# Kernel tuning notes

Hardware: AMD Instinct MI355X
Metric: run time of the kernel (lower is better)

Reference implementation:

```python
import jax, jax.numpy as jnp
import numpy as np

B, C_IN, C_OUT, H, W = 16, 128, 256, 80, 80
K, STRIDE, PAD = 3, 2, 1
KK = K * K
HO = (H + 2 * PAD - K) // STRIDE + 1
WO = (W + 2 * PAD - K) // STRIDE + 1


def setup_inputs() -> dict:
    key = jax.random.key(0)
    ks = jax.random.split(key, 3)
    x = jax.random.normal(ks[0], (B, C_IN, H, W), jnp.float32)
    offset_w = jax.random.normal(ks[1], (2 * KK, C_IN), jnp.float32) * 0.01
    offset_b = jnp.zeros((2 * KK,), jnp.float32)
    deform_w = jax.random.normal(ks[2], (C_OUT, C_IN, K, K), jnp.float32) * (1.0 / np.sqrt(C_IN * KK))
    deform_b = jnp.zeros((C_OUT,), jnp.float32)
    bn_gamma = jnp.ones((C_OUT,), jnp.float32)
    bn_beta = jnp.zeros((C_OUT,), jnp.float32)
    return dict(x=x, offset_w=offset_w, offset_b=offset_b, deform_w=deform_w,
                deform_b=deform_b, bn_gamma=bn_gamma, bn_beta=bn_beta)


def _bilinear_gather(x, py, px):
    # x: [B,C,H,W]; py,px: [B,KK,HO,WO] float sample coords; zero-pad outside.
    Bb, C, Hh, Ww = x.shape
    y0 = jnp.floor(py)
    x0 = jnp.floor(px)
    wy1 = py - y0
    wx1 = px - x0
    y0i = y0.astype(jnp.int32)
    x0i = x0.astype(jnp.int32)
    flat = x.reshape(Bb, C, Hh * Ww)

    def gather(yi, xi):
        valid = (yi >= 0) & (yi < Hh) & (xi >= 0) & (xi < Ww)
        idx = jnp.clip(yi, 0, Hh - 1) * Ww + jnp.clip(xi, 0, Ww - 1)
        g = jax.vmap(lambda f, i: f[:, i])(flat, idx.reshape(Bb, -1))
        g = g.reshape(Bb, C, *yi.shape[1:])
        return g * valid[:, None].astype(x.dtype)

    g00 = gather(y0i, x0i)
    g01 = gather(y0i, x0i + 1)
    g10 = gather(y0i + 1, x0i)
    g11 = gather(y0i + 1, x0i + 1)
    wy1 = wy1[:, None]  # [B,1,KK,HO,WO]
    wx1 = wx1[:, None]
    wy0 = 1.0 - wy1
    wx0 = 1.0 - wx1
    return wy0 * (wx0 * g00 + wx1 * g01) + wy1 * (wx0 * g10 + wx1 * g11)


def reference(x, offset_w, offset_b, deform_w, deform_b, bn_gamma, bn_beta):
    Bb = x.shape[0]
    # offset conv: 1x1, stride 2 (H,W even -> simple subsample)
    xs = x[:, :, ::2, ::2]  # [B,C,HO,WO]
    off = jnp.einsum('oc,bchw->bohw', offset_w, xs) + offset_b[None, :, None, None]
    off = off.reshape(Bb, KK, 2, HO, WO)  # torchvision layout: (dy,dx) per kernel tap
    dy, dx = off[:, :, 0], off[:, :, 1]
    ky = (jnp.arange(KK) // K).astype(jnp.float32)
    kx = (jnp.arange(KK) % K).astype(jnp.float32)
    base_y = (jnp.arange(HO) * STRIDE - PAD).astype(jnp.float32)
    base_x = (jnp.arange(WO) * STRIDE - PAD).astype(jnp.float32)
    py = base_y[None, None, :, None] + ky[None, :, None, None] + dy
    px = base_x[None, None, None, :] + kx[None, :, None, None] + dx
    sampled = _bilinear_gather(x, py, px)  # [B,C,KK,HO,WO]
    w = deform_w.reshape(C_OUT, C_IN * KK)
    out = jnp.einsum('ok,bkhw->bohw', w, sampled.reshape(Bb, C_IN * KK, HO, WO))
    out = out + deform_b[None, :, None, None]
    # BatchNorm2d in training mode (batch stats, biased var, eps=1e-5)
    mean = out.mean(axis=(0, 2, 3))
    var = out.var(axis=(0, 2, 3))
    out = (out - mean[None, :, None, None]) * jax.lax.rsqrt(var + 1e-5)[None, :, None, None]
    out = out * bn_gamma[None, :, None, None] + bn_beta[None, :, None, None]
    # SiLU
    return out * jax.nn.sigmoid(out)
```

## Files before the change

### kernel.cpp

```cpp
#include <hip/hip_runtime.h>
#include <hip/hip_bf16.h>

#define B_    16
#define CIN_  128
#define COUT_ 256
#define H_    80
#define W_    80
#define HO_   40
#define WO_   40
#define KK_   9
#define SK_   1152
#define NPIX_ 25600
#define NKS_  36

typedef __attribute__((ext_vector_type(8))) short short8;
typedef __attribute__((ext_vector_type(4))) float floatx4;

__device__ __forceinline__ unsigned short f2bu(float v) {
  __hip_bfloat16 h = __float2bfloat16(v);
  return *reinterpret_cast<unsigned short*>(&h);
}
__device__ __forceinline__ float bu2f(unsigned short u) {
  return __uint_as_float(((unsigned)u) << 16);
}
__device__ __forceinline__ unsigned int pk2(float a, float b) {
  return (unsigned)f2bu(a) | ((unsigned)f2bu(b) << 16);
}
__device__ __forceinline__ void gl_lds16(const unsigned short* g, unsigned short* l) {
  __builtin_amdgcn_global_load_lds(
      (const __attribute__((address_space(1))) unsigned int*)(const void*)g,
      (__attribute__((address_space(3))) unsigned int*)(void*)l, 16, 0, 0);
}

__global__ __launch_bounds__(256) void k_pack(const float* __restrict__ dw,
                                              unsigned short* __restrict__ Apk) {
  int t = blockIdx.x * 256 + threadIdx.x;
  int j  = t & 7;
  int qd = (t >> 3) & 3;
  int m  = (t >> 5) & 255;
  int ks = t >> 13;
  int k  = ks * 32 + qd * 8 + j;
  int kk = k >> 7, ci = k & 127;
  Apk[t] = f2bu(dw[m * SK_ + ci * KK_ + kk]);
}

__global__ __launch_bounds__(256) void k_cl(const float* __restrict__ x,
                                            const float* __restrict__ ow,
                                            const float* __restrict__ ob,
                                            unsigned short* __restrict__ xcl,
                                            float* __restrict__ off) {
  __shared__ unsigned int ts[CIN_ * 41];
  __shared__ float owl[18 * CIN_];
  __shared__ float obl[18];
  const int tid = threadIdx.x;
  const int bid = blockIdx.x;
  const int xcd = bid & 7;
  const int i0_ = bid >> 3;
  const int b   = (i0_ / 80) * 8 + xcd;
  const int y   = i0_ % 80;
  const bool even = (y & 1) == 0;

  for (int j = tid; j < CIN_ * 20; j += 256) {
    int ci = j / 20, xq = j % 20;
    float4 v = *(const float4*)&x[(((size_t)b * CIN_ + ci) * H_ + y) * W_ + xq * 4];
    ts[ci * 41 + xq * 2 + 0] = pk2(v.x, v.y);
    ts[ci * 41 + xq * 2 + 1] = pk2(v.z, v.w);
  }
  if (even) {
    for (int j = tid; j < 18 * CIN_; j += 256) owl[j] = ow[j];
    if (tid < 18) obl[tid] = ob[tid];
  }
  __syncthreads();

  unsigned short* op = xcl + ((size_t)b * H_ * W_ + (size_t)y * W_) * CIN_;
  for (int j = tid; j < 40 * 32; j += 256) {
    int xw = j >> 5, cg = j & 31;
    unsigned w0 = ts[(cg * 4 + 0) * 41 + xw];
    unsigned w1 = ts[(cg * 4 + 1) * 41 + xw];
    unsigned w2 = ts[(cg * 4 + 2) * 41 + xw];
    unsigned w3 = ts[(cg * 4 + 3) * 41 + xw];
    uint2 lo = make_uint2((w0 & 0xFFFFu) | (w1 << 16),
                          (w2 & 0xFFFFu) | (w3 << 16));
    uint2 hi = make_uint2((w0 >> 16) | (w1 & 0xFFFF0000u),
                          (w2 >> 16) | (w3 & 0xFFFF0000u));
    *(uint2*)(op + (size_t)(2 * xw) * CIN_ + cg * 4)     = lo;
    *(uint2*)(op + (size_t)(2 * xw + 1) * CIN_ + cg * 4) = hi;
  }

  if (even) {
    const int ho = y >> 1;
    for (int i = tid; i < 18 * WO_; i += 256) {
      int o = i / WO_, wo = i - o * WO_;
      float acc = obl[o];
      const float* wr = &owl[o * CIN_];
#pragma unroll 4
      for (int ci = 0; ci < CIN_; ci++)
        acc += wr[ci] * bu2f((unsigned short)(ts[ci * 41 + wo] & 0xFFFFu));
      off[((b * 18 + o) * HO_ + ho) * WO_ + wo] = acc;
    }
  }
}

__global__ __launch_bounds__(256) void k_sample_cl(const unsigned short* __restrict__ xcl,
                                                   const float* __restrict__ off,
                                                   unsigned short* __restrict__ Spk) {
  __shared__ __align__(16) int   pidx[80 * 4];
  __shared__ __align__(16) float pw[80 * 4];
  const int tid = threadIdx.x;
  const int j0   = blockIdx.x;
  const int xcd  = j0 & 7;
  const int s    = j0 >> 3;
  const int b_hi = s / 180;
  const int t0   = s % 180;
  const int g    = t0 / 9;
  const int kk   = t0 % 9;
  const int b    = b_hi * 8 + xcd;
  const int ho0  = g * 2;

  if (tid < 80) {
    int hop = tid / 40, px = tid % 40;
    int ho = ho0 + hop;
    float dy = off[((b * 18 + 2 * kk) * HO_ + ho) * WO_ + px];
    float dx = off[((b * 18 + 2 * kk + 1) * HO_ + ho) * WO_ + px];
    float py  = (float)(2 * ho - 1 + (kk / 3)) + dy;
    float pxf = (float)(2 * px - 1 + (kk % 3)) + dx;
    float y0f = floorf(py), x0f = floorf(pxf);
    float wy1 = py - y0f, wx1 = pxf - x0f;
    float wy0 = 1.f - wy1, wx0 = 1.f - wx1;
    int y0 = (int)y0f, x0 = (int)x0f;
    int y1 = y0 + 1, x1 = x0 + 1;
    bool vy0 = (y0 >= 0) && (y0 < H_);
    bool vy1 = (y1 >= 0) && (y1 < H_);
    bool vx0 = (x0 >= 0) && (x0 < W_);
    bool vx1 = (x1 >= 0) && (x1 < W_);
    int y0c = min(max(y0, 0), H_ - 1), y1c = min(max(y1, 0), H_ - 1);
    int x0c = min(max(x0, 0), W_ - 1), x1c = min(max(x1, 0), W_ - 1);
    pidx[tid * 4 + 0] = (y0c * W_ + x0c) << 7;  pw[tid * 4 + 0] = (vy0 && vx0) ? wy0 * wx0 : 0.f;
    pidx[tid * 4 + 1] = (y0c * W_ + x1c) << 7;  pw[tid * 4 + 1] = (vy0 && vx1) ? wy0 * wx1 : 0.f;
    pidx[tid * 4 + 2] = (y1c * W_ + x0c) << 7;  pw[tid * 4 + 2] = (vy1 && vx0) ? wy1 * wx0 : 0.f;
    pidx[tid * 4 + 3] = (y1c * W_ + x1c) << 7;  pw[tid * 4 + 3] = (vy1 && vx1) ? wy1 * wx1 : 0.f;
  }
  __syncthreads();

  const unsigned short* xb = xcl + (size_t)b * (H_ * W_ * CIN_);
#pragma unroll
  for (int it = 0; it < 5; it++) {
    int i = it * 256 + tid;
    int oct = i & 15;
    int pxh = i >> 4;
    int4   I  = *(const int4*)&pidx[pxh * 4];
    float4 Wv = *(const float4*)&pw[pxh * 4];
    short8 c00 = *(const short8*)(xb + I.x + oct * 8);
    short8 c01 = *(const short8*)(xb + I.y + oct * 8);
    short8 c10 = *(const short8*)(xb + I.z + oct * 8);
    short8 c11 = *(const short8*)(xb + I.w + oct * 8);
    short8 r;
#pragma unroll
    for (int i2 = 0; i2 < 8; i2++) {
      float v = Wv.x * bu2f((unsigned short)c00[i2]) +
                Wv.y * bu2f((unsigned short)c01[i2]) +
                Wv.z * bu2f((unsigned short)c10[i2]) +
                Wv.w * bu2f((unsigned short)c11[i2]);
      r[i2] = (short)f2bu(v);
    }
    int p  = b * 1600 + (ho0 + (pxh / 40)) * 40 + (pxh % 40);
    int pt = p >> 4, lm = p & 15;
    int ks = kk * 4 + (oct >> 2);
    int qd = oct & 3;
    *(short8*)&Spk[(((size_t)pt * NKS_ + ks) * 64 + qd * 16 + lm) * 8] = r;
  }
}

__global__ __launch_bounds__(256) void k_gemm(const unsigned short* __restrict__ Apk,
                                              const unsigned short* __restrict__ Spk,
                                              float* __restrict__ c0,
                                              float* __restrict__ c1) {
  __shared__ __align__(16) unsigned short a_sh[2][2048];
  __shared__ __align__(16) unsigned short b_sh[2][2048];

  const int tid = threadIdx.x;
  const int wv = tid >> 6;
  const int ln = tid & 63;
  const int lm = ln & 15;
  const int qd = ln >> 4;

  const int bid = blockIdx.x;
  const int xcd = bid & 7;
  const int i   = bid >> 3;
  const int b   = xcd + 8 * (i / 200);
  const int r_  = i % 200;
  const int pxg = r_ >> 3;
  const int cq  = (r_ >> 1) & 3;
  const int ksp = r_ & 1;
  const int pt0 = b * 100 + pxg * 4;
  const int cbase = cq * 64;
  const int ks0 = ksp * 18;

  const unsigned short* agbase = Apk + (size_t)ks0 * 8192 + cbase * 32 + tid * 8;
  const unsigned short* bgbase = Spk + ((size_t)(pt0 + wv) * NKS_ + ks0) * 512 + ln * 8;

  floatx4 acc[4];
#pragma unroll
  for (int mt = 0; mt < 4; mt++) acc[mt] = (floatx4){0.f, 0.f, 0.f, 0.f};

  gl_lds16(agbase, &a_sh[0][0] + wv * 512);
  gl_lds16(bgbase, &b_sh[0][0] + wv * 512);
  __syncthreads();

  for (int ks = 0; ks < 18; ks++) {
    const int buf = ks & 1, nb = buf ^ 1;
    if (ks + 1 < 18) {
      gl_lds16(agbase + (size_t)(ks + 1) * 8192, &a_sh[nb][0] + wv * 512);
      gl_lds16(bgbase + (size_t)(ks + 1) * 512,  &b_sh[nb][0] + wv * 512);
    }
    const unsigned short* al = &a_sh[buf][0] + lm * 32 + qd * 8;
    const unsigned short* bl = &b_sh[buf][0] + wv * 512 + ln * 8;
    short8 a0 = *(const short8*)(al + 0 * 512);
    short8 a1 = *(const short8*)(al + 1 * 512);
    short8 a2 = *(const short8*)(al + 2 * 512);
    short8 a3 = *(const short8*)(al + 3 * 512);
    short8 bv = *(const short8*)(bl);
    acc[0] = __builtin_amdgcn_mfma_f32_16x16x32_bf16(a0, bv, acc[0], 0, 0, 0);
    acc[1] = __builtin_amdgcn_mfma_f32_16x16x32_bf16(a1, bv, acc[1], 0, 0, 0);
    acc[2] = __builtin_amdgcn_mfma_f32_16x16x32_bf16(a2, bv, acc[2], 0, 0, 0);
    acc[3] = __builtin_amdgcn_mfma_f32_16x16x32_bf16(a3, bv, acc[3], 0, 0, 0);
    __syncthreads();
  }

  const int p = (pt0 + wv) * 16 + lm;
  const int bb = p / 1600, rem = p % 1600;
  float* ob = (ksp ? c1 : c0) + (size_t)bb * COUT_ * 1600 + rem;
#pragma unroll
  for (int mt = 0; mt < 4; mt++) {
#pragma unroll
    for (int r = 0; r < 4; r++) {
      const int c = cbase + mt * 16 + qd * 4 + r;
      ob[(size_t)c * 1600] = acc[mt][r];
    }
  }
}

__global__ __launch_bounds__(256) void k_stats(const float* __restrict__ io0,
                                               const float* __restrict__ io1,
                                               float* __restrict__ accum) {
  const int c = blockIdx.x >> 2;
  const int q = blockIdx.x & 3;
  const int tid = threadIdx.x;
  float s1 = 0.f, s2 = 0.f;
  for (int i = q * (NPIX_ / 4) + tid; i < (q + 1) * (NPIX_ / 4); i += 256) {
    int b = i / 1600, r = i - b * 1600;
    size_t idx = ((size_t)b * COUT_ + c) * 1600 + r;
    float v = io0[idx] + io1[idx];
    s1 += v;
    s2 += v * v;
  }
#pragma unroll
  for (int d = 1; d < 64; d <<= 1) {
    s1 += __shfl_xor(s1, d, 64);
    s2 += __shfl_xor(s2, d, 64);
  }
  __shared__ float rs[4], rq[4];
  if ((tid & 63) == 0) { rs[tid >> 6] = s1; rq[tid >> 6] = s2; }
  __syncthreads();
  if (tid == 0) {
    atomicAdd(&accum[c],         rs[0] + rs[1] + rs[2] + rs[3]);
    atomicAdd(&accum[COUT_ + c], rq[0] + rq[1] + rq[2] + rq[3]);
  }
}

__global__ __launch_bounds__(256) void k_bn(float* __restrict__ io0,
                                            const float* __restrict__ io1,
                                            const float* __restrict__ accum,
                                            const float* __restrict__ gamma,
                                            const float* __restrict__ beta) {
  const int t = blockIdx.x * 256 + threadIdx.x;
  const int i0 = t * 4;
  const int c = (i0 / (HO_ * WO_)) % COUT_;
  const float mean = accum[c] * (1.f / NPIX_);
  const float var  = accum[COUT_ + c] * (1.f / NPIX_) - mean * mean;
  const float inv  = rsqrtf(var + 1e-5f);
  const float g  = gamma[c] * inv;
  const float be = beta[c] - mean * g;
  float4 r0 = *(const float4*)(io0 + i0);
  float4 r1 = *(const float4*)(io1 + i0);
  float v[4] = {r0.x + r1.x, r0.y + r1.y, r0.z + r1.z, r0.w + r1.w};
#pragma unroll
  for (int q = 0; q < 4; q++) {
    float u = v[q] * g + be;
    v[q] = u / (1.f + expf(-u));
  }
  *(float4*)(io0 + i0) = make_float4(v[0], v[1], v[2], v[3]);
}

extern "C" void kernel_launch(void* const* d_in, const int* in_sizes, int n_in,
                              void* d_out, int out_size, void* d_ws, size_t ws_size,
                              hipStream_t stream) {
  const float* x     = (const float*)d_in[0];
  const float* ow    = (const float*)d_in[1];
  const float* ob    = (const float*)d_in[2];
  const float* dw    = (const float*)d_in[3];
  const float* gamma = (const float*)d_in[5];
  const float* beta  = (const float*)d_in[6];
  float* out = (float*)d_out;

  float* off   = (float*)d_ws;
  float* accum = off + B_ * 18 * HO_ * WO_;
  unsigned short* Apk = (unsigned short*)(accum + 2 * COUT_);
  unsigned short* Spk = Apk + (size_t)SK_ * COUT_;
  unsigned short* xcl = Spk + (size_t)NPIX_ * SK_;
  float* c1 = (float*)xcl;

  hipMemsetAsync(accum, 0, 2 * COUT_ * sizeof(float), stream);
  k_pack<<<SK_, 256, 0, stream>>>(dw, Apk);
  k_cl<<<B_ * H_, 256, 0, stream>>>(x, ow, ob, xcl, off);
  k_sample_cl<<<B_ * KK_ * 20, 256, 0, stream>>>(xcl, off, Spk);
  k_gemm<<<3200, 256, 0, stream>>>(Apk, Spk, out, c1);
  k_stats<<<COUT_ * 4, 256, 0, stream>>>(out, c1, accum);
  k_bn<<<(NPIX_ * COUT_ / 4 + 255) / 256, 256, 0, stream>>>(
      out, c1, accum, gamma, beta);
}
```

Before: 195.2 us.

## Drop split-K, widen GEMM channel tile, fuse BN statistics into GEMM epilogue

The GEMM no longer splits K across two partial outputs. Each block now covers 128 output channels over the full K range, with 8 MFMA accumulators per wave, and the grid shrinks from 3200 to 800 blocks. The per-channel sum and sum-of-squares are reduced in the GEMM epilogue through shuffles, LDS atomics and global atomics, so the separate stats kernel and the second partial buffer go away. This removes a full read/write pass of the output and the partial-sum traffic, at the cost of fewer blocks (lower occupancy and parallelism), longer K loops and more atomics.

```diff
diff --git a/kernel.cpp b/kernel.cpp
--- a/kernel.cpp
+++ b/kernel.cpp
@@ -173,9 +173,9 @@
 
 __global__ __launch_bounds__(256) void k_gemm(const unsigned short* __restrict__ Apk,
                                               const unsigned short* __restrict__ Spk,
-                                              float* __restrict__ c0,
-                                              float* __restrict__ c1) {
-  __shared__ __align__(16) unsigned short a_sh[2][2048];
+                                              float* __restrict__ out,
+                                              float* __restrict__ accum) {
+  __shared__ __align__(16) unsigned short a_sh[2][4096];
   __shared__ __align__(16) unsigned short b_sh[2][2048];
 
   const int tid = threadIdx.x;
@@ -187,89 +187,83 @@
   const int bid = blockIdx.x;
   const int xcd = bid & 7;
   const int i   = bid >> 3;
-  const int b   = xcd + 8 * (i / 200);
-  const int r_  = i % 200;
-  const int pxg = r_ >> 3;
-  const int cq  = (r_ >> 1) & 3;
-  const int ksp = r_ & 1;
+  const int b   = xcd + 8 * (i / 50);
+  const int r_  = i % 50;
+  const int pxg = r_ >> 1;
+  const int cq  = r_ & 1;
   const int pt0 = b * 100 + pxg * 4;
-  const int cbase = cq * 64;
-  const int ks0 = ksp * 18;
-
-  const unsigned short* agbase = Apk + (size_t)ks0 * 8192 + cbase * 32 + tid * 8;
-  const unsigned short* bgbase = Spk + ((size_t)(pt0 + wv) * NKS_ + ks0) * 512 + ln * 8;
-
-  floatx4 acc[4];
-#pragma unroll
-  for (int mt = 0; mt < 4; mt++) acc[mt] = (floatx4){0.f, 0.f, 0.f, 0.f};
-
-  gl_lds16(agbase, &a_sh[0][0] + wv * 512);
-  gl_lds16(bgbase, &b_sh[0][0] + wv * 512);
-  __syncthreads();
-
-  for (int ks = 0; ks < 18; ks++) {
+  const int cbase = cq * 128;
+
+  const unsigned short* agbase = Apk + cbase * 32 + tid * 8;
+  const unsigned short* bgbase = Spk + ((size_t)(pt0 + wv) * NKS_) * 512 + ln * 8;
+
+  floatx4 acc[8];
+#pragma unroll
+  for (int mt = 0; mt < 8; mt++) acc[mt] = (floatx4){0.f, 0.f, 0.f, 0.f};
+
+  gl_lds16(agbase,        &a_sh[0][0]    + wv * 512);
+  gl_lds16(agbase + 2048, &a_sh[0][2048] + wv * 512);
+  gl_lds16(bgbase,        &b_sh[0][0]    + wv * 512);
+  __syncthreads();
+
+  for (int ks = 0; ks < NKS_; ks++) {
     const int buf = ks & 1, nb = buf ^ 1;
-    if (ks + 1 < 18) {
-      gl_lds16(agbase + (size_t)(ks + 1) * 8192, &a_sh[nb][0] + wv * 512);
-      gl_lds16(bgbase + (size_t)(ks + 1) * 512,  &b_sh[nb][0] + wv * 512);
+    if (ks + 1 < NKS_) {
+      gl_lds16(agbase + (size_t)(ks + 1) * 8192,        &a_sh[nb][0]    + wv * 512);
+      gl_lds16(agbase + (size_t)(ks + 1) * 8192 + 2048, &a_sh[nb][2048] + wv * 512);
+      gl_lds16(bgbase + (size_t)(ks + 1) * 512,         &b_sh[nb][0]    + wv * 512);
     }
     const unsigned short* al = &a_sh[buf][0] + lm * 32 + qd * 8;
-    const unsigned short* bl = &b_sh[buf][0] + wv * 512 + ln * 8;
-    short8 a0 = *(const short8*)(al + 0 * 512);
-    short8 a1 = *(const short8*)(al + 1 * 512);
-    short8 a2 = *(const short8*)(al + 2 * 512);
-    short8 a3 = *(const short8*)(al + 3 * 512);
-    short8 bv = *(const short8*)(bl);
-    acc[0] = __builtin_amdgcn_mfma_f32_16x16x32_bf16(a0, bv, acc[0], 0, 0, 0);
-    acc[1] = __builtin_amdgcn_mfma_f32_16x16x32_bf16(a1, bv, acc[1], 0, 0, 0);
-    acc[2] = __builtin_amdgcn_mfma_f32_16x16x32_bf16(a2, bv, acc[2], 0, 0, 0);
-    acc[3] = __builtin_amdgcn_mfma_f32_16x16x32_bf16(a3, bv, acc[3], 0, 0, 0);
+    short8 bv = *(const short8*)(&b_sh[buf][0] + wv * 512 + ln * 8);
+#pragma unroll
+    for (int mt = 0; mt < 8; mt++) {
+      short8 av = *(const short8*)(al + mt * 512);
+      acc[mt] = __builtin_amdgcn_mfma_f32_16x16x32_bf16(av, bv, acc[mt], 0, 0, 0);
+    }
     __syncthreads();
   }
 
   const int p = (pt0 + wv) * 16 + lm;
   const int bb = p / 1600, rem = p % 1600;
-  float* ob = (ksp ? c1 : c0) + (size_t)bb * COUT_ * 1600 + rem;
-#pragma unroll
-  for (int mt = 0; mt < 4; mt++) {
+  float* ob = out + (size_t)bb * COUT_ * 1600 + rem;
+#pragma unroll
+  for (int mt = 0; mt < 8; mt++) {
 #pragma unroll
     for (int r = 0; r < 4; r++) {
       const int c = cbase + mt * 16 + qd * 4 + r;
       ob[(size_t)c * 1600] = acc[mt][r];
     }
   }
-}
-
-__global__ __launch_bounds__(256) void k_stats(const float* __restrict__ io0,
-                                               const float* __restrict__ io1,
-                                               float* __restrict__ accum) {
-  const int c = blockIdx.x >> 2;
-  const int q = blockIdx.x & 3;
-  const int tid = threadIdx.x;
-  float s1 = 0.f, s2 = 0.f;
-  for (int i = q * (NPIX_ / 4) + tid; i < (q + 1) * (NPIX_ / 4); i += 256) {
-    int b = i / 1600, r = i - b * 1600;
-    size_t idx = ((size_t)b * COUT_ + c) * 1600 + r;
-    float v = io0[idx] + io1[idx];
-    s1 += v;
-    s2 += v * v;
-  }
-#pragma unroll
-  for (int d = 1; d < 64; d <<= 1) {
-    s1 += __shfl_xor(s1, d, 64);
-    s2 += __shfl_xor(s2, d, 64);
-  }
-  __shared__ float rs[4], rq[4];
-  if ((tid & 63) == 0) { rs[tid >> 6] = s1; rq[tid >> 6] = s2; }
-  __syncthreads();
-  if (tid == 0) {
-    atomicAdd(&accum[c],         rs[0] + rs[1] + rs[2] + rs[3]);
-    atomicAdd(&accum[COUT_ + c], rq[0] + rq[1] + rq[2] + rq[3]);
+
+  float* red = (float*)&a_sh[0][0];
+  red[tid < 256 ? tid : 0] = 0.f;
+  __syncthreads();
+#pragma unroll
+  for (int mt = 0; mt < 8; mt++) {
+#pragma unroll
+    for (int r = 0; r < 4; r++) {
+      float s = acc[mt][r];
+      float q = s * s;
+#pragma unroll
+      for (int d = 1; d < 16; d <<= 1) {
+        s += __shfl_xor(s, d, 16);
+        q += __shfl_xor(q, d, 16);
+      }
+      if (lm == 0) {
+        int lc = mt * 16 + qd * 4 + r;
+        atomicAdd(&red[lc], s);
+        atomicAdd(&red[128 + lc], q);
+      }
+    }
+  }
+  __syncthreads();
+  if (tid < 128) {
+    atomicAdd(&accum[cbase + tid],         red[tid]);
+    atomicAdd(&accum[COUT_ + cbase + tid], red[128 + tid]);
   }
 }
 
 __global__ __launch_bounds__(256) void k_bn(float* __restrict__ io0,
-                                            const float* __restrict__ io1,
                                             const float* __restrict__ accum,
                                             const float* __restrict__ gamma,
                                             const float* __restrict__ beta) {
@@ -282,8 +276,7 @@
   const float g  = gamma[c] * inv;
   const float be = beta[c] - mean * g;
   float4 r0 = *(const float4*)(io0 + i0);
-  float4 r1 = *(const float4*)(io1 + i0);
-  float v[4] = {r0.x + r1.x, r0.y + r1.y, r0.z + r1.z, r0.w + r1.w};
+  float v[4] = {r0.x, r0.y, r0.z, r0.w};
 #pragma unroll
   for (int q = 0; q < 4; q++) {
     float u = v[q] * g + be;
@@ -308,14 +301,12 @@
   unsigned short* Apk = (unsigned short*)(accum + 2 * COUT_);
   unsigned short* Spk = Apk + (size_t)SK_ * COUT_;
   unsigned short* xcl = Spk + (size_t)NPIX_ * SK_;
-  float* c1 = (float*)xcl;
 
   hipMemsetAsync(accum, 0, 2 * COUT_ * sizeof(float), stream);
   k_pack<<<SK_, 256, 0, stream>>>(dw, Apk);
   k_cl<<<B_ * H_, 256, 0, stream>>>(x, ow, ob, xcl, off);
   k_sample_cl<<<B_ * KK_ * 20, 256, 0, stream>>>(xcl, off, Spk);
-  k_gemm<<<3200, 256, 0, stream>>>(Apk, Spk, out, c1);
-  k_stats<<<COUT_ * 4, 256, 0, stream>>>(out, c1, accum);
+  k_gemm<<<800, 256, 0, stream>>>(Apk, Spk, out, accum);
   k_bn<<<(NPIX_ * COUT_ / 4 + 255) / 256, 256, 0, stream>>>(
-      out, c1, accum, gamma, beta);
-}
+      out, accum, gamma, beta);
+}
```

After: 197.9 us. About the same (+1.4%).
